# Kernel tuning notes

Measured on AMD Instinct MI355X. Metric: run time of the kernel, lower is better.

Reference implementation:

```python
import jax, jax.numpy as jnp
import numpy as np

HID = 1024       # hidden_size
H = 8            # num_attention_heads
KVH = 2          # num_key_value_heads
D = HID // H     # head_dim = 128
WINDOW = 2048    # sliding_window
THETA = 10000.0  # rope_theta
B, S = 1, 4096


def rotate_half(x):
    x1, x2 = jnp.split(x, 2, axis=-1)
    return jnp.concatenate([-x2, x1], axis=-1)


def setup_inputs() -> dict:
    key = jax.random.key(0)
    ks = jax.random.split(key, 5)
    scale = 0.02
    return {
        "hidden_states": jax.random.normal(ks[0], (B, S, HID), dtype=jnp.float32),
        "wq": jax.random.normal(ks[1], (H * D, HID), dtype=jnp.float32) * scale,
        "wk": jax.random.normal(ks[2], (KVH * D, HID), dtype=jnp.float32) * scale,
        "wv": jax.random.normal(ks[3], (KVH * D, HID), dtype=jnp.float32) * scale,
        "wo": jax.random.normal(ks[4], (HID, H * D), dtype=jnp.float32) * scale,
        "position_ids": jnp.broadcast_to(jnp.arange(S, dtype=jnp.int64 if jax.config.jax_enable_x64 else jnp.int32)[None, :], (B, S)),
    }


def reference(hidden_states, wq, wk, wv, wo, position_ids):
    b, s, _ = hidden_states.shape
    # projections (torch nn.Linear: x @ W^T)
    q = (hidden_states @ wq.T).reshape(b, s, H, D).transpose(0, 2, 1, 3)      # bhsd
    k = (hidden_states @ wk.T).reshape(b, s, KVH, D).transpose(0, 2, 1, 3)    # b(kv)sd
    v = (hidden_states @ wv.T).reshape(b, s, KVH, D).transpose(0, 2, 1, 3)

    # RoPE cache (head_dim, seq_len)
    inv_freq = 1.0 / THETA ** (jnp.arange(0, D, 2, dtype=jnp.float32) / D)
    t = jnp.arange(s, dtype=jnp.float32)
    freqs = t[:, None] * inv_freq[None, :]
    emb = jnp.concatenate([freqs, freqs], axis=-1)           # (S, D)
    cos = jnp.cos(emb)[position_ids][:, None]                # (B,1,S,D)
    sin = jnp.sin(emb)[position_ids][:, None]
    q = q * cos + rotate_half(q) * sin
    k = k * cos + rotate_half(k) * sin

    # GQA: repeat kv heads to match query heads (repeat_interleave on head dim)
    groups = H // KVH
    k = jnp.repeat(k, groups, axis=1)
    v = jnp.repeat(v, groups, axis=1)

    # full score matrix with sliding-window causal mask
    scores = jnp.einsum("bhqd,bhkd->bhqk", q, k)
    i = jnp.arange(s)[:, None]
    j = jnp.arange(s)[None, :]
    mask = (j <= i) & (j > i - WINDOW)                       # causal + window
    scores = jnp.where(mask[None, None], scores, -jnp.inf) / jnp.sqrt(jnp.float32(D))

    probs = jax.nn.softmax(scores.astype(jnp.float32), axis=-1).astype(q.dtype)
    ctx = jnp.einsum("bhqk,bhkd->bhqd", probs, v)
    ctx = ctx.transpose(0, 2, 1, 3).reshape(b, s, H * D)
    return ctx @ wo.T
```

## Files before the change

kernel.cpp:

```cpp
#include <hip/hip_runtime.h>

#define S_LEN 4096
#define HIDDEN 1024
#define NH 8
#define NKV 2
#define HD 128
#define WIN 2048

typedef short bf16x8 __attribute__((ext_vector_type(8)));
typedef float f32x4 __attribute__((ext_vector_type(4)));
typedef unsigned short u16x4 __attribute__((ext_vector_type(4)));

__device__ __forceinline__ unsigned short f2b(float f) {
    unsigned int u = __builtin_bit_cast(unsigned int, f);
    u += 0x7fffu + ((u >> 16) & 1u);
    return (unsigned short)(u >> 16);
}
__device__ __forceinline__ float b2f(unsigned short u) {
    unsigned int x = ((unsigned int)u) << 16;
    return __builtin_bit_cast(float, x);
}

__device__ __forceinline__ void gl_lds16(const unsigned short* g, unsigned short* l) {
    __builtin_amdgcn_global_load_lds(
        (const __attribute__((address_space(1))) unsigned int*)g,
        (__attribute__((address_space(3))) unsigned int*)l, 16, 0, 0);
}

#define WAIT_VM8   0x0F78
#define WAIT_VM0   0x0F70
#define WAIT_LGKM0 0xC07F

__global__ __launch_bounds__(256) void cvt5(
    const float* __restrict__ s0, unsigned short* __restrict__ t0, int n0,
    const float* __restrict__ s1, unsigned short* __restrict__ t1, int n1,
    const float* __restrict__ s2, unsigned short* __restrict__ t2, int n2,
    const float* __restrict__ s3, unsigned short* __restrict__ t3, int n3,
    const float* __restrict__ s4, unsigned short* __restrict__ t4, int n4)
{
    int i = blockIdx.x * 256 + threadIdx.x;
    const float* s; unsigned short* t;
    if (i < n0)              { s = s0; t = t0; }
    else if ((i -= n0) < n1) { s = s1; t = t1; }
    else if ((i -= n1) < n2) { s = s2; t = t2; }
    else if ((i -= n2) < n3) { s = s3; t = t3; }
    else if ((i -= n3) < n4) { s = s4; t = t4; }
    else return;
    f32x4 v = *(const f32x4*)(s + (size_t)i * 4);
    u16x4 r = { f2b(v[0]), f2b(v[1]), f2b(v[2]), f2b(v[3]) };
    *(u16x4*)(t + (size_t)i * 4) = r;
}

__global__ __launch_bounds__(256, 2) void gemm128(
    const unsigned short* __restrict__ A, const unsigned short* __restrict__ W,
    float* __restrict__ Cf, unsigned short* __restrict__ Cb,
    int M, int N, int K)
{
    __shared__ alignas(16) unsigned short As[128 * 32];
    __shared__ alignas(16) unsigned short Bs[128 * 32];

    int lane = threadIdx.x & 63;
    int w = threadIdx.x >> 6;
    int l15 = lane & 15, quad = lane >> 4;

    int tiles_n = N >> 7;
    int mt0 = (int)blockIdx.x / tiles_n;
    int nt0 = (int)blockIdx.x - mt0 * tiles_n;

    size_t goffA[2], goffB[2];
    #pragma unroll
    for (int is = 0; is < 2; ++is) {
        int s = w * 128 + is * 64 + lane;
        int row = s >> 2, spos = s & 3;
        int kblk = spos ^ ((row >> 1) & 3);
        goffA[is] = (size_t)(mt0 * 128 + row) * K + kblk * 8;
        goffB[is] = (size_t)(nt0 * 128 + row) * K + kblk * 8;
    }
    unsigned short* dstA0 = As + (w * 128 + 0) * 8;
    unsigned short* dstA1 = As + (w * 128 + 64) * 8;
    unsigned short* dstB0 = Bs + (w * 128 + 0) * 8;
    unsigned short* dstB1 = Bs + (w * 128 + 64) * 8;

    int arow0 = (w >> 1) * 64;
    int brow0 = (w & 1) * 64;
    int aoff[4], boff[4];
    #pragma unroll
    for (int t = 0; t < 4; ++t) {
        int ra = arow0 + t * 16 + l15;
        aoff[t] = (ra * 4 + (quad ^ ((ra >> 1) & 3))) * 8;
        int rb = brow0 + t * 16 + l15;
        boff[t] = (rb * 4 + (quad ^ ((rb >> 1) & 3))) * 8;
    }

    f32x4 acc[4][4];
    #pragma unroll
    for (int i = 0; i < 4; ++i)
        #pragma unroll
        for (int j = 0; j < 4; ++j) acc[i][j] = (f32x4){0.f, 0.f, 0.f, 0.f};

    for (int k0 = 0; k0 < K; k0 += 32) {
        gl_lds16(A + goffA[0] + k0, dstA0);
        gl_lds16(A + goffA[1] + k0, dstA1);
        gl_lds16(W + goffB[0] + k0, dstB0);
        gl_lds16(W + goffB[1] + k0, dstB1);
        __syncthreads();

        bf16x8 af[4], bf_[4];
        #pragma unroll
        for (int t = 0; t < 4; ++t) {
            af[t]  = *(const bf16x8*)(As + aoff[t]);
            bf_[t] = *(const bf16x8*)(Bs + boff[t]);
        }
        #pragma unroll
        for (int i = 0; i < 4; ++i)
            #pragma unroll
            for (int j = 0; j < 4; ++j)
                acc[i][j] = __builtin_amdgcn_mfma_f32_16x16x32_bf16(af[i], bf_[j], acc[i][j], 0, 0, 0);
        __syncthreads();
    }

    #pragma unroll
    for (int i = 0; i < 4; ++i) {
        int row0 = mt0 * 128 + arow0 + i * 16 + quad * 4;
        #pragma unroll
        for (int j = 0; j < 4; ++j) {
            int col = nt0 * 128 + brow0 + j * 16 + l15;
            if (Cf) {
                #pragma unroll
                for (int reg = 0; reg < 4; ++reg)
                    Cf[(size_t)(row0 + reg) * N + col] = acc[i][j][reg];
            } else {
                #pragma unroll
                for (int reg = 0; reg < 4; ++reg)
                    Cb[(size_t)(row0 + reg) * N + col] = f2b(acc[i][j][reg]);
            }
        }
    }
}

#define QKVW (HIDDEN + 2 * NKV * HD)
__global__ __launch_bounds__(256) void rope_convert(
    const unsigned short* __restrict__ X, const int* __restrict__ pos,
    unsigned short* __restrict__ Qb, unsigned short* __restrict__ Kb,
    unsigned short* __restrict__ Vt)
{
    const float qscale = 0.08838834764831843f;
    int tid = blockIdx.x * 256 + threadIdx.x;
    int s = tid / (12 * 64);
    int r = tid - s * (12 * 64);
    int slot = r >> 6;
    int d = r & 63;
    if (s >= S_LEN) return;

    if (slot < 10) {
        bool is64 = (pos[1] == 0) && (pos[3] == 0);
        int pv = is64 ? pos[2 * s] : pos[s];
        float p = (float)pv;
        float inv = exp2f(-(float)d * (13.287712379549449f / 64.0f));
        float ang = p * inv;
        float c = cosf(ang), sn = sinf(ang);
        if (slot < 8) {
            size_t src = (size_t)s * QKVW + slot * HD + d;
            size_t dst = (size_t)s * HIDDEN + slot * HD + d;
            float x1 = b2f(X[src]), x2 = b2f(X[src + 64]);
            Qb[dst]      = f2b((x1 * c - x2 * sn) * qscale);
            Qb[dst + 64] = f2b((x2 * c + x1 * sn) * qscale);
        } else {
            int kvh = slot - 8;
            size_t src = (size_t)s * QKVW + HIDDEN + kvh * HD + d;
            size_t dst = (size_t)kvh * S_LEN * HD + (size_t)s * HD + d;
            float x1 = b2f(X[src]), x2 = b2f(X[src + 64]);
            Kb[dst]      = f2b(x1 * c - x2 * sn);
            Kb[dst + 64] = f2b(x2 * c + x1 * sn);
        }
    } else {
        int kvh = slot - 10;
        size_t src = (size_t)s * QKVW + HIDDEN + NKV * HD + kvh * HD + d;
        Vt[(size_t)(kvh * HD + d) * S_LEN + s]      = X[src];
        Vt[(size_t)(kvh * HD + d + 64) * S_LEN + s] = X[src + 64];
    }
}

__global__ __launch_bounds__(256, 2) void attn_coop(
    const unsigned short* __restrict__ Qb, const unsigned short* __restrict__ Kb,
    const unsigned short* __restrict__ Vt, unsigned short* __restrict__ Ctx)
{
    __shared__ alignas(16) unsigned short Klds[2][64 * 128];
    __shared__ alignas(16) unsigned short Vlds[2][128 * 64];
    __shared__ alignas(16) unsigned short Plds[4][16 * 72];

    int lane = threadIdx.x & 63;
    int w = threadIdx.x >> 6;
    int l15 = lane & 15, quad = lane >> 4;
    int h = blockIdx.y;
    int kv = h >> 2;
    int qb = blockIdx.x * 64;
    int q16 = qb + w * 16;

    bf16x8 a_q[4];
    const unsigned short* qrow = Qb + (size_t)(q16 + l15) * HIDDEN + h * HD + quad * 8;
    #pragma unroll
    for (int st = 0; st < 4; ++st) a_q[st] = *(const bf16x8*)(qrow + st * 32);

    bf16x8 b_one;
    #pragma unroll
    for (int i = 0; i < 8; ++i) b_one[i] = (short)0x3F80;

    int lo = qb + 63 - (WIN - 1); if (lo < 0) lo = 0; lo &= ~63;
    int nch = (qb + 64 - lo) >> 6;

    const unsigned short* gbase;
    unsigned short* ldsdst[2];
    int myoff[8];
    int jmul;
    if (w < 2) {
        gbase = Kb + (size_t)kv * S_LEN * HD;
        ldsdst[0] = &Klds[0][w * 8 * 512];
        ldsdst[1] = &Klds[1][w * 8 * 512];
        jmul = HD;
        #pragma unroll
        for (int tt = 0; tt < 8; ++tt) {
            int t = w * 8 + tt;
            int key  = t * 4 + (lane >> 4);
            int dblk = (lane & 15) ^ (key & 15);
            myoff[tt] = key * HD + dblk * 8;
        }
    } else {
        gbase = Vt + (size_t)kv * HD * S_LEN;
        ldsdst[0] = &Vlds[0][(w - 2) * 8 * 512];
        ldsdst[1] = &Vlds[1][(w - 2) * 8 * 512];
        jmul = 1;
        #pragma unroll
        for (int tt = 0; tt < 8; ++tt) {
            int t = (w - 2) * 8 + tt;
            int d    = t * 8 + (lane >> 3);
            int kblk = (lane & 7) ^ (d & 7);
            myoff[tt] = d * S_LEN + kblk * 8;
        }
    }

    auto issue = [&](int c) {
        int j0 = lo + c * 64;
        const unsigned short* src = gbase + (size_t)j0 * jmul;
        unsigned short* dst = ldsdst[c & 1];
        #pragma unroll
        for (int tt = 0; tt < 8; ++tt)
            gl_lds16(src + myoff[tt], dst + tt * 512);
    };

    f32x4 o[9];
    #pragma unroll
    for (int nd = 0; nd < 9; ++nd) o[nd] = (f32x4){0.f, 0.f, 0.f, 0.f};

    unsigned short* pw = &Plds[w][0];

    issue(0);

    for (int c = 0; c < nch; ++c) {
        int j0 = lo + c * 64;
        const unsigned short* Kc = &Klds[c & 1][0];
        const unsigned short* Vc = &Vlds[c & 1][0];

        if (c + 1 < nch) {
            issue(c + 1);
            __asm__ volatile("" ::: "memory");
            __builtin_amdgcn_s_waitcnt(WAIT_VM8);
        } else {
            __asm__ volatile("" ::: "memory");
            __builtin_amdgcn_s_waitcnt(WAIT_VM0);
        }
        __builtin_amdgcn_s_barrier();
        __asm__ volatile("" ::: "memory");

        f32x4 sc[4];
        #pragma unroll
        for (int t = 0; t < 4; ++t) {
            sc[t] = (f32x4){0.f, 0.f, 0.f, 0.f};
            int key = t * 16 + l15;
            #pragma unroll
            for (int st = 0; st < 4; ++st) {
                int off16 = key * 16 + ((st * 4 + quad) ^ (key & 15));
                bf16x8 bk = *(const bf16x8*)(Kc + off16 * 8);
                sc[t] = __builtin_amdgcn_mfma_f32_16x16x32_bf16(a_q[st], bk, sc[t], 0, 0, 0);
            }
        }

        float p[4][4];
        if (j0 + 63 <= q16 && j0 > q16 + 15 - WIN) {
            #pragma unroll
            for (int t = 0; t < 4; ++t)
                #pragma unroll
                for (int reg = 0; reg < 4; ++reg) p[t][reg] = __expf(sc[t][reg]);
        } else {
            #pragma unroll
            for (int t = 0; t < 4; ++t) {
                int jj = j0 + t * 16 + l15;
                #pragma unroll
                for (int reg = 0; reg < 4; ++reg) {
                    int i = q16 + quad * 4 + reg;
                    p[t][reg] = (jj <= i && jj > i - WIN) ? __expf(sc[t][reg]) : 0.f;
                }
            }
        }

        #pragma unroll
        for (int t = 0; t < 4; ++t)
            #pragma unroll
            for (int reg = 0; reg < 4; ++reg)
                pw[(quad * 4 + reg) * 72 + t * 16 + l15] = f2b(p[t][reg]);

        __builtin_amdgcn_wave_barrier();
        __builtin_amdgcn_s_waitcnt(WAIT_LGKM0);
        __builtin_amdgcn_wave_barrier();

        bf16x8 a_p0 = *(const bf16x8*)(pw + l15 * 72 + quad * 8);
        bf16x8 a_p1 = *(const bf16x8*)(pw + l15 * 72 + 32 + quad * 8);

        #pragma unroll
        for (int nd = 0; nd < 8; ++nd) {
            int d = nd * 16 + l15;
            int o16a = d * 8 + ((quad) ^ (d & 7));
            int o16b = d * 8 + ((4 + quad) ^ (d & 7));
            bf16x8 bv0 = *(const bf16x8*)(Vc + o16a * 8);
            bf16x8 bv1 = *(const bf16x8*)(Vc + o16b * 8);
            o[nd] = __builtin_amdgcn_mfma_f32_16x16x32_bf16(a_p0, bv0, o[nd], 0, 0, 0);
            o[nd] = __builtin_amdgcn_mfma_f32_16x16x32_bf16(a_p1, bv1, o[nd], 0, 0, 0);
        }
        o[8] = __builtin_amdgcn_mfma_f32_16x16x32_bf16(a_p0, b_one, o[8], 0, 0, 0);
        o[8] = __builtin_amdgcn_mfma_f32_16x16x32_bf16(a_p1, b_one, o[8], 0, 0, 0);

        __asm__ volatile("" ::: "memory");
        __builtin_amdgcn_s_waitcnt(WAIT_LGKM0);
        __builtin_amdgcn_s_barrier();
        __asm__ volatile("" ::: "memory");
    }

    #pragma unroll
    for (int nd = 0; nd < 8; ++nd) {
        int d = nd * 16 + l15;
        #pragma unroll
        for (int reg = 0; reg < 4; ++reg) {
            int q = q16 + quad * 4 + reg;
            Ctx[(size_t)q * HIDDEN + h * HD + d] = f2b(o[nd][reg] / o[8][reg]);
        }
    }
}

extern "C" void kernel_launch(void* const* d_in, const int* in_sizes, int n_in,
                              void* d_out, int out_size, void* d_ws, size_t ws_size,
                              hipStream_t stream)
{
    const float* hidden = (const float*)d_in[0];
    const float* wq = (const float*)d_in[1];
    const float* wk = (const float*)d_in[2];
    const float* wv = (const float*)d_in[3];
    const float* wo = (const float*)d_in[4];
    const int* pos = (const int*)d_in[5];
    float* out = (float*)d_out;

    char* ws = (char*)d_ws;
    size_t off = 0;
    unsigned short* Hb   = (unsigned short*)(ws + off); off += (size_t)S_LEN * HIDDEN * 2;
    unsigned short* Wqkv = (unsigned short*)(ws + off); off += (size_t)QKVW * HIDDEN * 2;
    unsigned short* Wob  = (unsigned short*)(ws + off); off += (size_t)HIDDEN * HIDDEN * 2;
    unsigned short* XQKV = (unsigned short*)(ws + off); off += (size_t)S_LEN * QKVW * 2;
    unsigned short* Qb   = (unsigned short*)(ws + off); off += (size_t)S_LEN * HIDDEN * 2;
    unsigned short* Kb   = (unsigned short*)(ws + off); off += (size_t)S_LEN * NKV * HD * 2;
    unsigned short* Vt   = (unsigned short*)(ws + off); off += (size_t)S_LEN * NKV * HD * 2;
    unsigned short* Cb   = (unsigned short*)(ws + off); off += (size_t)S_LEN * HIDDEN * 2;

    const int n_h  = S_LEN * HIDDEN / 4;
    const int n_wq = HIDDEN * HIDDEN / 4;
    const int n_wk = NKV * HD * HIDDEN / 4;
    int tot4 = n_h + n_wq + 2 * n_wk + n_wq;
    cvt5<<<(tot4 + 255) / 256, 256, 0, stream>>>(
        hidden, Hb, n_h,
        wq, Wqkv, n_wq,
        wk, Wqkv + (size_t)HIDDEN * HIDDEN, n_wk,
        wv, Wqkv + (size_t)(HIDDEN + NKV * HD) * HIDDEN, n_wk,
        wo, Wob, n_wq);

    gemm128<<<(S_LEN / 128) * (QKVW / 128), 256, 0, stream>>>(
        Hb, Wqkv, nullptr, XQKV, S_LEN, QKVW, HIDDEN);

    rope_convert<<<S_LEN * 12 * 64 / 256, 256, 0, stream>>>(
        XQKV, pos, Qb, Kb, Vt);

    attn_coop<<<dim3(S_LEN / 64, NH), 256, 0, stream>>>(Qb, Kb, Vt, Cb);

    gemm128<<<(S_LEN / 128) * (HIDDEN / 128), 256, 0, stream>>>(
        Cb, Wob, out, nullptr, S_LEN, HIDDEN, HIDDEN);
}
```

Baseline: 200.7 us.

## Fuse RoPE into QKV GEMM epilogue, split V transpose, software-pipeline attention loop

The QKV projection now applies RoPE and the Q scaling directly in its epilogue. Partner columns are exchanged through shared memory, which removes the intermediate XQKV buffer and the separate rope_convert pass. V is written row-major and transposed by a small tiled LDS kernel. The attention loop is restructured so the PV product for chunk c-1 overlaps the score computation for chunk c, and the K/V loads are split so each half of the waves fetches a different stage. This trades a more complex epilogue, with extra LDS and syncs, for less global traffic and better overlap of MFMA work.

New measurement: 194.2 us. -3.2%, faster.

```diff
diff --git a/kernel.cpp b/kernel.cpp
--- a/kernel.cpp
+++ b/kernel.cpp
@@ -139,45 +139,167 @@
 }
 
 #define QKVW (HIDDEN + 2 * NKV * HD)
-__global__ __launch_bounds__(256) void rope_convert(
-    const unsigned short* __restrict__ X, const int* __restrict__ pos,
+__global__ __launch_bounds__(256, 2) void gemmqkv(
+    const unsigned short* __restrict__ A, const unsigned short* __restrict__ W,
+    const int* __restrict__ pos,
     unsigned short* __restrict__ Qb, unsigned short* __restrict__ Kb,
-    unsigned short* __restrict__ Vt)
+    unsigned short* __restrict__ Vg)
 {
+    __shared__ alignas(16) unsigned short As[128 * 32];
+    __shared__ alignas(16) unsigned short Bs[128 * 32];
+    __shared__ float Ex[4][32][68];
+
+    int lane = threadIdx.x & 63;
+    int w = threadIdx.x >> 6;
+    int l15 = lane & 15, quad = lane >> 4;
+
+    const int K = HIDDEN;
+    int mt0 = (int)blockIdx.x / 12;
+    int nt0 = (int)blockIdx.x - mt0 * 12;
+
+    size_t goffA[2], goffB[2];
+    #pragma unroll
+    for (int is = 0; is < 2; ++is) {
+        int s = w * 128 + is * 64 + lane;
+        int row = s >> 2, spos = s & 3;
+        int kblk = spos ^ ((row >> 1) & 3);
+        goffA[is] = (size_t)(mt0 * 128 + row) * K + kblk * 8;
+        goffB[is] = (size_t)(nt0 * 128 + row) * K + kblk * 8;
+    }
+    unsigned short* dstA0 = As + (w * 128 + 0) * 8;
+    unsigned short* dstA1 = As + (w * 128 + 64) * 8;
+    unsigned short* dstB0 = Bs + (w * 128 + 0) * 8;
+    unsigned short* dstB1 = Bs + (w * 128 + 64) * 8;
+
+    int arow0 = (w >> 1) * 64;
+    int brow0 = (w & 1) * 64;
+    int aoff[4], boff[4];
+    #pragma unroll
+    for (int t = 0; t < 4; ++t) {
+        int ra = arow0 + t * 16 + l15;
+        aoff[t] = (ra * 4 + (quad ^ ((ra >> 1) & 3))) * 8;
+        int rb = brow0 + t * 16 + l15;
+        boff[t] = (rb * 4 + (quad ^ ((rb >> 1) & 3))) * 8;
+    }
+
+    f32x4 acc[4][4];
+    #pragma unroll
+    for (int i = 0; i < 4; ++i)
+        #pragma unroll
+        for (int j = 0; j < 4; ++j) acc[i][j] = (f32x4){0.f, 0.f, 0.f, 0.f};
+
+    for (int k0 = 0; k0 < K; k0 += 32) {
+        gl_lds16(A + goffA[0] + k0, dstA0);
+        gl_lds16(A + goffA[1] + k0, dstA1);
+        gl_lds16(W + goffB[0] + k0, dstB0);
+        gl_lds16(W + goffB[1] + k0, dstB1);
+        __syncthreads();
+
+        bf16x8 af[4], bf_[4];
+        #pragma unroll
+        for (int t = 0; t < 4; ++t) {
+            af[t]  = *(const bf16x8*)(As + aoff[t]);
+            bf_[t] = *(const bf16x8*)(Bs + boff[t]);
+        }
+        #pragma unroll
+        for (int i = 0; i < 4; ++i)
+            #pragma unroll
+            for (int j = 0; j < 4; ++j)
+                acc[i][j] = __builtin_amdgcn_mfma_f32_16x16x32_bf16(af[i], bf_[j], acc[i][j], 0, 0, 0);
+        __syncthreads();
+    }
+
+    if (nt0 >= 10) {
+        int kv = nt0 - 10;
+        #pragma unroll
+        for (int i = 0; i < 4; ++i) {
+            int row0 = mt0 * 128 + arow0 + i * 16 + quad * 4;
+            #pragma unroll
+            for (int j = 0; j < 4; ++j) {
+                int col = kv * 128 + brow0 + j * 16 + l15;
+                #pragma unroll
+                for (int reg = 0; reg < 4; ++reg)
+                    Vg[(size_t)(row0 + reg) * (NKV * HD) + col] = f2b(acc[i][j][reg]);
+            }
+        }
+        return;
+    }
+
+    bool isQ = (nt0 < 8);
+    int kv = nt0 - 8;
+    bool is64 = (pos[1] == 0) && (pos[3] == 0);
     const float qscale = 0.08838834764831843f;
-    int tid = blockIdx.x * 256 + threadIdx.x;
-    int s = tid / (12 * 64);
-    int r = tid - s * (12 * 64);
-    int slot = r >> 6;
-    int d = r & 63;
-    if (s >= S_LEN) return;
-
-    if (slot < 10) {
-        bool is64 = (pos[1] == 0) && (pos[3] == 0);
-        int pv = is64 ? pos[2 * s] : pos[s];
-        float p = (float)pv;
-        float inv = exp2f(-(float)d * (13.287712379549449f / 64.0f));
-        float ang = p * inv;
-        float c = cosf(ang), sn = sinf(ang);
-        if (slot < 8) {
-            size_t src = (size_t)s * QKVW + slot * HD + d;
-            size_t dst = (size_t)s * HIDDEN + slot * HD + d;
-            float x1 = b2f(X[src]), x2 = b2f(X[src + 64]);
-            Qb[dst]      = f2b((x1 * c - x2 * sn) * qscale);
-            Qb[dst + 64] = f2b((x2 * c + x1 * sn) * qscale);
-        } else {
-            int kvh = slot - 8;
-            size_t src = (size_t)s * QKVW + HIDDEN + kvh * HD + d;
-            size_t dst = (size_t)kvh * S_LEN * HD + (size_t)s * HD + d;
-            float x1 = b2f(X[src]), x2 = b2f(X[src + 64]);
-            Kb[dst]      = f2b(x1 * c - x2 * sn);
-            Kb[dst + 64] = f2b(x2 * c + x1 * sn);
-        }
-    } else {
-        int kvh = slot - 10;
-        size_t src = (size_t)s * QKVW + HIDDEN + NKV * HD + kvh * HD + d;
-        Vt[(size_t)(kvh * HD + d) * S_LEN + s]      = X[src];
-        Vt[(size_t)(kvh * HD + d + 64) * S_LEN + s] = X[src + 64];
+
+    float invf[4];
+    #pragma unroll
+    for (int j = 0; j < 4; ++j) {
+        int d6 = (brow0 + j * 16 + l15) & 63;
+        invf[j] = exp2f(-(float)d6 * (13.287712379549449f / 64.0f));
+    }
+
+    #pragma unroll
+    for (int r2 = 0; r2 < 2; ++r2) {
+        #pragma unroll
+        for (int ii = 0; ii < 2; ++ii) {
+            int i = r2 * 2 + ii;
+            #pragma unroll
+            for (int j = 0; j < 4; ++j)
+                #pragma unroll
+                for (int reg = 0; reg < 4; ++reg)
+                    Ex[w][ii * 16 + quad * 4 + reg][j * 16 + l15] = acc[i][j][reg];
+        }
+        __syncthreads();
+        #pragma unroll
+        for (int ii = 0; ii < 2; ++ii) {
+            int i = r2 * 2 + ii;
+            #pragma unroll
+            for (int reg = 0; reg < 4; ++reg) {
+                int s = mt0 * 128 + arow0 + i * 16 + quad * 4 + reg;
+                int pv_ = is64 ? pos[2 * s] : pos[s];
+                float pf = (float)pv_;
+                #pragma unroll
+                for (int j = 0; j < 4; ++j) {
+                    float sn, cs;
+                    __sincosf(pf * invf[j], &sn, &cs);
+                    float a  = acc[i][j][reg];
+                    float pr = Ex[w ^ 1][ii * 16 + quad * 4 + reg][j * 16 + l15];
+                    int d_local = brow0 + j * 16 + l15;
+                    float outv = (d_local < 64) ? (a * cs - pr * sn) : (a * cs + pr * sn);
+                    if (isQ) {
+                        Qb[(size_t)s * HIDDEN + nt0 * HD + d_local] = f2b(outv * qscale);
+                    } else {
+                        Kb[(size_t)kv * S_LEN * HD + (size_t)s * HD + d_local] = f2b(outv);
+                    }
+                }
+            }
+        }
+        __syncthreads();
+    }
+}
+
+__global__ __launch_bounds__(256) void vtrans(
+    const unsigned short* __restrict__ Vg, unsigned short* __restrict__ Vt)
+{
+    __shared__ unsigned short L[64][66];
+    int st = (int)blockIdx.x >> 2, dt = (int)blockIdx.x & 3;
+    int s0 = st * 64, d0 = dt * 64;
+    int tid = threadIdx.x;
+    {
+        int dl = tid & 63, sl4 = tid >> 6;
+        #pragma unroll
+        for (int p = 0; p < 16; ++p) {
+            int sl = p * 4 + sl4;
+            L[sl][dl] = Vg[(size_t)(s0 + sl) * (NKV * HD) + d0 + dl];
+        }
+    }
+    __syncthreads();
+    {
+        int sl = tid & 63, dl4 = tid >> 6;
+        #pragma unroll
+        for (int p = 0; p < 16; ++p) {
+            int dl = p * 4 + dl4;
+            Vt[(size_t)(d0 + dl) * S_LEN + s0 + sl] = L[sl][dl];
+        }
     }
 }
 
@@ -254,24 +376,8 @@
 
     unsigned short* pw = &Plds[w][0];
 
-    issue(0);
-
-    for (int c = 0; c < nch; ++c) {
+    auto do_scores = [&](int c, const unsigned short* Kc) {
         int j0 = lo + c * 64;
-        const unsigned short* Kc = &Klds[c & 1][0];
-        const unsigned short* Vc = &Vlds[c & 1][0];
-
-        if (c + 1 < nch) {
-            issue(c + 1);
-            __asm__ volatile("" ::: "memory");
-            __builtin_amdgcn_s_waitcnt(WAIT_VM8);
-        } else {
-            __asm__ volatile("" ::: "memory");
-            __builtin_amdgcn_s_waitcnt(WAIT_VM0);
-        }
-        __builtin_amdgcn_s_barrier();
-        __asm__ volatile("" ::: "memory");
-
         f32x4 sc[4];
         #pragma unroll
         for (int t = 0; t < 4; ++t) {
@@ -284,7 +390,6 @@
                 sc[t] = __builtin_amdgcn_mfma_f32_16x16x32_bf16(a_q[st], bk, sc[t], 0, 0, 0);
             }
         }
-
         float p[4][4];
         if (j0 + 63 <= q16 && j0 > q16 + 15 - WIN) {
             #pragma unroll
@@ -302,20 +407,17 @@
                 }
             }
         }
-
         #pragma unroll
         for (int t = 0; t < 4; ++t)
             #pragma unroll
             for (int reg = 0; reg < 4; ++reg)
                 pw[(quad * 4 + reg) * 72 + t * 16 + l15] = f2b(p[t][reg]);
-
-        __builtin_amdgcn_wave_barrier();
-        __builtin_amdgcn_s_waitcnt(WAIT_LGKM0);
-        __builtin_amdgcn_wave_barrier();
-
+    };
+
+    auto do_pv = [&](int cm1) {
         bf16x8 a_p0 = *(const bf16x8*)(pw + l15 * 72 + quad * 8);
         bf16x8 a_p1 = *(const bf16x8*)(pw + l15 * 72 + 32 + quad * 8);
-
+        const unsigned short* Vc = &Vlds[cm1 & 1][0];
         #pragma unroll
         for (int nd = 0; nd < 8; ++nd) {
             int d = nd * 16 + l15;
@@ -328,12 +430,51 @@
         }
         o[8] = __builtin_amdgcn_mfma_f32_16x16x32_bf16(a_p0, b_one, o[8], 0, 0, 0);
         o[8] = __builtin_amdgcn_mfma_f32_16x16x32_bf16(a_p1, b_one, o[8], 0, 0, 0);
+    };
+
+    if (w < 2) issue(0);
+
+    {
+        if (1 < nch) {
+            if (w < 2) issue(1); else issue(0);
+            __asm__ volatile("" ::: "memory");
+            __builtin_amdgcn_s_waitcnt(WAIT_VM8);
+        } else {
+            if (w >= 2) issue(0);
+            __asm__ volatile("" ::: "memory");
+            __builtin_amdgcn_s_waitcnt(WAIT_VM0);
+        }
+        __builtin_amdgcn_s_barrier();
+        __asm__ volatile("" ::: "memory");
+        do_scores(0, &Klds[0][0]);
+        __builtin_amdgcn_s_waitcnt(WAIT_LGKM0);
+        __builtin_amdgcn_s_barrier();
+        __asm__ volatile("" ::: "memory");
+    }
+
+    for (int c = 1; c < nch; ++c) {
+        if (c + 1 < nch) {
+            if (w < 2) issue(c + 1); else issue(c);
+            __asm__ volatile("" ::: "memory");
+            __builtin_amdgcn_s_waitcnt(WAIT_VM8);
+        } else {
+            if (w >= 2) issue(c);
+            __asm__ volatile("" ::: "memory");
+            __builtin_amdgcn_s_waitcnt(WAIT_VM0);
+        }
+        __builtin_amdgcn_s_barrier();
+        __asm__ volatile("" ::: "memory");
+
+        do_pv(c - 1);
+        do_scores(c, &Klds[c & 1][0]);
 
         __asm__ volatile("" ::: "memory");
         __builtin_amdgcn_s_waitcnt(WAIT_LGKM0);
         __builtin_amdgcn_s_barrier();
         __asm__ volatile("" ::: "memory");
     }
+
+    do_pv(nch - 1);
 
     #pragma unroll
     for (int nd = 0; nd < 8; ++nd) {
@@ -363,9 +504,9 @@
     unsigned short* Hb   = (unsigned short*)(ws + off); off += (size_t)S_LEN * HIDDEN * 2;
     unsigned short* Wqkv = (unsigned short*)(ws + off); off += (size_t)QKVW * HIDDEN * 2;
     unsigned short* Wob  = (unsigned short*)(ws + off); off += (size_t)HIDDEN * HIDDEN * 2;
-    unsigned short* XQKV = (unsigned short*)(ws + off); off += (size_t)S_LEN * QKVW * 2;
     unsigned short* Qb   = (unsigned short*)(ws + off); off += (size_t)S_LEN * HIDDEN * 2;
     unsigned short* Kb   = (unsigned short*)(ws + off); off += (size_t)S_LEN * NKV * HD * 2;
+    unsigned short* Vg   = (unsigned short*)(ws + off); off += (size_t)S_LEN * NKV * HD * 2;
     unsigned short* Vt   = (unsigned short*)(ws + off); off += (size_t)S_LEN * NKV * HD * 2;
     unsigned short* Cb   = (unsigned short*)(ws + off); off += (size_t)S_LEN * HIDDEN * 2;
 
@@ -380,11 +521,10 @@
         wv, Wqkv + (size_t)(HIDDEN + NKV * HD) * HIDDEN, n_wk,
         wo, Wob, n_wq);
 
-    gemm128<<<(S_LEN / 128) * (QKVW / 128), 256, 0, stream>>>(
-        Hb, Wqkv, nullptr, XQKV, S_LEN, QKVW, HIDDEN);
-
-    rope_convert<<<S_LEN * 12 * 64 / 256, 256, 0, stream>>>(
-        XQKV, pos, Qb, Kb, Vt);
+    gemmqkv<<<(S_LEN / 128) * 12, 256, 0, stream>>>(
+        Hb, Wqkv, pos, Qb, Kb, Vg);
+
+    vtrans<<<(S_LEN / 64) * ((NKV * HD) / 64), 256, 0, stream>>>(Vg, Vt);
 
     attn_coop<<<dim3(S_LEN / 64, NH), 256, 0, stream>>>(Qb, Kb, Vt, Cb);
 
```
